# Performance work log

Measured on AMD Instinct MI355X. Metric: run time of the kernel, lower is better.

The kernel has to match this reference:

```python
import jax, jax.numpy as jnp
import numpy as np

ROWS, COLS, DIM, BATCH = 128, 128, 64, 128

def setup_inputs() -> dict:
    key = jax.random.key(0)
    kx, kw = jax.random.split(key)
    x = jax.random.normal(kx, (BATCH, DIM), dtype=jnp.float32)
    # SOM codebook weights, randomly initialized as in _initialize_weights()
    weights = jax.random.normal(kw, (ROWS, COLS, DIM), dtype=jnp.float32)
    return {"x": x, "weights": weights}

def reference(x, weights):
    # Squared Euclidean distance from each input to every grid neuron.
    # x: (B, D); weights: (R, C, D) -> distances: (B, R, C)
    diff = weights[None, :, :, :] - x[:, None, None, :]
    distances = jnp.sum(diff * diff, axis=-1)
    return distances
```

## Files before the change

kernel.cpp:

```cpp
#include <hip/hip_runtime.h>


#define SOM_B   128
#define SOM_D   64
#define SOM_N   16384
#define SOM_BT  16
#define SOM_TPB 256

__global__ __launch_bounds__(SOM_TPB, 2)
void som_dist_kernel(const float* __restrict__ x,
                     const float* __restrict__ w,
                     float* __restrict__ out) {
    __shared__ float xs[SOM_BT][SOM_D];
    __shared__ float x2s[SOM_BT];

    const int tid = threadIdx.x;
    const int n   = blockIdx.x * SOM_TPB + tid;
    const int b0  = blockIdx.y * SOM_BT;

    {
        const float4* xg = (const float4*)(x + (size_t)b0 * SOM_D);
        ((float4*)&xs[0][0])[tid] = xg[tid];
    }
    __syncthreads();

    if (tid < SOM_BT) {
        float s = 0.f;
        #pragma unroll
        for (int d = 0; d < SOM_D; ++d) {
            float v = xs[tid][d];
            s += v * v;
        }
        x2s[tid] = s;
    }

    float4 wr[16];
    {
        const float4* wg = (const float4*)(w + (size_t)n * SOM_D);
        #pragma unroll
        for (int i = 0; i < 16; ++i) wr[i] = wg[i];
    }
    float wn2 = 0.f;
    #pragma unroll
    for (int i = 0; i < 16; ++i) {
        wn2 += wr[i].x * wr[i].x + wr[i].y * wr[i].y
             + wr[i].z * wr[i].z + wr[i].w * wr[i].w;
    }

    __syncthreads();

    #pragma unroll
    for (int b = 0; b < SOM_BT; ++b) {
        const float4* xrow = (const float4*)&xs[b][0];
        float acc = 0.f;
        #pragma unroll
        for (int i = 0; i < 16; ++i) {
            float4 xv = xrow[i];
            acc += wr[i].x * xv.x + wr[i].y * xv.y
                 + wr[i].z * xv.z + wr[i].w * xv.w;
        }
        float res = wn2 + x2s[b] - 2.f * acc;
        out[(size_t)(b0 + b) * SOM_N + n] = res;
    }
}

extern "C" void kernel_launch(void* const* d_in, const int* in_sizes, int n_in,
                              void* d_out, int out_size, void* d_ws, size_t ws_size,
                              hipStream_t stream) {
    const float* x = (const float*)d_in[0];
    const float* w = (const float*)d_in[1];
    float* out = (float*)d_out;

    dim3 grid(SOM_N / SOM_TPB, SOM_B / SOM_BT);
    dim3 block(SOM_TPB);
    som_dist_kernel<<<grid, block, 0, stream>>>(x, w, out);
}
```

Measured before the change: 68.73 us.

## Transpose codebook in a prep kernel for coalesced loads, read x from global

After: 77.33 us. 1.13x slower.

```diff
diff --git a/kernel.cpp b/kernel.cpp
--- a/kernel.cpp
+++ b/kernel.cpp
@@ -7,60 +7,71 @@
 #define SOM_BT  16
 #define SOM_TPB 256
 
+__global__ __launch_bounds__(SOM_TPB)
+void som_prep(const float* __restrict__ x,
+              const float* __restrict__ w,
+              float4* __restrict__ wt,
+              float* __restrict__ x2) {
+    const int tid = threadIdx.x;
+    const int j   = blockIdx.x * SOM_TPB + tid;
+    const int i   = j >> 14;
+    const int n   = j & (SOM_N - 1);
+    const float4* w4 = (const float4*)w;
+    wt[j] = w4[(n << 4) | i];
+
+    if (blockIdx.x < SOM_B && tid < 64) {
+        float v = x[(blockIdx.x << 6) + tid];
+        float s = v * v;
+        #pragma unroll
+        for (int off = 32; off > 0; off >>= 1)
+            s += __shfl_down(s, off, 64);
+        if (tid == 0) x2[blockIdx.x] = s;
+    }
+}
+
 __global__ __launch_bounds__(SOM_TPB, 2)
-void som_dist_kernel(const float* __restrict__ x,
-                     const float* __restrict__ w,
-                     float* __restrict__ out) {
-    __shared__ float xs[SOM_BT][SOM_D];
-    __shared__ float x2s[SOM_BT];
-
+void som_main(const float* __restrict__ x,
+              const float4* __restrict__ wt,
+              const float* __restrict__ x2,
+              float* __restrict__ out) {
     const int tid = threadIdx.x;
     const int n   = blockIdx.x * SOM_TPB + tid;
     const int b0  = blockIdx.y * SOM_BT;
 
-    {
-        const float4* xg = (const float4*)(x + (size_t)b0 * SOM_D);
-        ((float4*)&xs[0][0])[tid] = xg[tid];
-    }
-    __syncthreads();
+    float4 wr[16];
+    #pragma unroll
+    for (int i = 0; i < 16; ++i) wr[i] = wt[(i << 14) + n];
 
-    if (tid < SOM_BT) {
-        float s = 0.f;
-        #pragma unroll
-        for (int d = 0; d < SOM_D; ++d) {
-            float v = xs[tid][d];
-            s += v * v;
-        }
-        x2s[tid] = s;
-    }
-
-    float4 wr[16];
-    {
-        const float4* wg = (const float4*)(w + (size_t)n * SOM_D);
-        #pragma unroll
-        for (int i = 0; i < 16; ++i) wr[i] = wg[i];
-    }
     float wn2 = 0.f;
     #pragma unroll
-    for (int i = 0; i < 16; ++i) {
+    for (int i = 0; i < 16; ++i)
         wn2 += wr[i].x * wr[i].x + wr[i].y * wr[i].y
              + wr[i].z * wr[i].z + wr[i].w * wr[i].w;
-    }
 
-    __syncthreads();
+    const float4* x4 = (const float4*)x;
+    float* op = out + (size_t)b0 * SOM_N + n;
 
     #pragma unroll
     for (int b = 0; b < SOM_BT; ++b) {
-        const float4* xrow = (const float4*)&xs[b][0];
-        float acc = 0.f;
+        const float4* xb = x4 + ((b0 + b) << 4);
+        float a0 = 0.f, a1 = 0.f, a2 = 0.f, a3 = 0.f;
         #pragma unroll
-        for (int i = 0; i < 16; ++i) {
-            float4 xv = xrow[i];
-            acc += wr[i].x * xv.x + wr[i].y * xv.y
-                 + wr[i].z * xv.z + wr[i].w * xv.w;
+        for (int i = 0; i < 16; i += 4) {
+            float4 xv0 = xb[i + 0];
+            float4 xv1 = xb[i + 1];
+            float4 xv2 = xb[i + 2];
+            float4 xv3 = xb[i + 3];
+            a0 += wr[i + 0].x * xv0.x + wr[i + 0].y * xv0.y
+                + wr[i + 0].z * xv0.z + wr[i + 0].w * xv0.w;
+            a1 += wr[i + 1].x * xv1.x + wr[i + 1].y * xv1.y
+                + wr[i + 1].z * xv1.z + wr[i + 1].w * xv1.w;
+            a2 += wr[i + 2].x * xv2.x + wr[i + 2].y * xv2.y
+                + wr[i + 2].z * xv2.z + wr[i + 2].w * xv2.w;
+            a3 += wr[i + 3].x * xv3.x + wr[i + 3].y * xv3.y
+                + wr[i + 3].z * xv3.z + wr[i + 3].w * xv3.w;
         }
-        float res = wn2 + x2s[b] - 2.f * acc;
-        out[(size_t)(b0 + b) * SOM_N + n] = res;
+        float acc = (a0 + a1) + (a2 + a3);
+        op[(size_t)b * SOM_N] = fmaf(-2.f, acc, wn2 + x2[b0 + b]);
     }
 }
 
@@ -71,7 +82,9 @@
     const float* w = (const float*)d_in[1];
     float* out = (float*)d_out;
 
-    dim3 grid(SOM_N / SOM_TPB, SOM_B / SOM_BT);
-    dim3 block(SOM_TPB);
-    som_dist_kernel<<<grid, block, 0, stream>>>(x, w, out);
+    float4* wt = (float4*)d_ws;
+    float*  x2 = (float*)((char*)d_ws + SOM_N * SOM_D * 4);
+
+    som_prep<<<dim3((SOM_N * SOM_D / 4) / SOM_TPB), dim3(SOM_TPB), 0, stream>>>(x, w, wt, x2);
+    som_main<<<dim3(SOM_N / SOM_TPB, SOM_B / SOM_BT), dim3(SOM_TPB), 0, stream>>>(x, wt, x2, out);
 }
```
